# Kernel optimization log

Measured on AMD Instinct MI355X. Metric: run time of the kernel, lower is better.

## Reference

```python
import jax, jax.numpy as jnp
import numpy as np

B, S, D, H = 4, 2048, 1024, 16
DK = D // H

def setup_inputs() -> dict:
    key = jax.random.key(0)
    ks = jax.random.split(key, 11)
    s = 1.0 / np.sqrt(D)
    inp = {
        'q': jax.random.normal(ks[0], (B, S, D), jnp.float32),
        'k': jax.random.normal(ks[1], (B, S, D), jnp.float32),
        'v': jax.random.normal(ks[2], (B, S, D), jnp.float32),
        'Wq': jax.random.normal(ks[3], (D, D), jnp.float32) * s,
        'bq': jnp.zeros((D,), jnp.float32),
        'Wk': jax.random.normal(ks[4], (D, D), jnp.float32) * s,
        'bk': jnp.zeros((D,), jnp.float32),
        'Wv': jax.random.normal(ks[5], (D, D), jnp.float32) * s,
        'bv': jnp.zeros((D,), jnp.float32),
        'Wo': jax.random.normal(ks[6], (D, D), jnp.float32) * s,
        'bo': jnp.zeros((D,), jnp.float32),
    }
    return inp

def reference(q, k, v, Wq, bq, Wk, bk, Wv, bv, Wo, bo):
    # torch Linear: x @ W.T + b
    def proj(x, W, b):
        # [B,S,D] -> [B,H,S,DK]
        y = jnp.einsum('bsd,ed->bse', x, W) + b
        return y.reshape(B, S, H, DK).transpose(0, 2, 1, 3)
    qh, kh, vh = proj(q, Wq, bq), proj(k, Wk, bk), proj(v, Wv, bv)
    scores = jnp.einsum('bhqd,bhkd->bhqk', qh, kh) / jnp.sqrt(jnp.float32(DK))
    attn = jax.nn.softmax(scores, axis=-1)  # dropout p=0.0 (eval)
    out = jnp.einsum('bhqk,bhkd->bhqd', attn, vh)
    concat = out.transpose(0, 2, 1, 3).reshape(B, S, D)
    return jnp.einsum('bsd,ed->bse', concat, Wo) + bo
```

## Files before the change

kernel.cpp:

```cpp
#include <hip/hip_runtime.h>
#include <hip/hip_bf16.h>
#include <cstdint>

#define BB 4
#define SS 2048
#define DD 1024
#define HH 16
#define DKH 64

using bf16x8  = __attribute__((ext_vector_type(8))) __bf16;
using f32x4   = __attribute__((ext_vector_type(4))) float;
using ushort8 = __attribute__((ext_vector_type(8))) unsigned short;

__device__ __forceinline__ unsigned short f2bf(float f) {
  unsigned int u = __builtin_bit_cast(unsigned int, f);
  u += 0x7fffu + ((u >> 16) & 1u);
  return (unsigned short)(u >> 16);
}

__device__ __forceinline__ void gload16(const void* g, void* l) {
  __builtin_amdgcn_global_load_lds(
      (const __attribute__((address_space(1))) void*)g,
      (__attribute__((address_space(3))) void*)l,
      16, 0, 0);
}

__global__ __launch_bounds__(256) void cvt_one(const float* __restrict__ s,
                                               unsigned short* __restrict__ d) {
  const int i = ((int)blockIdx.x * 256 + (int)threadIdx.x) * 8;
  const float4* p = reinterpret_cast<const float4*>(s + i);
  float4 x = p[0], y = p[1];
  ushort8 r;
  r[0] = f2bf(x.x); r[1] = f2bf(x.y); r[2] = f2bf(x.z); r[3] = f2bf(x.w);
  r[4] = f2bf(y.x); r[5] = f2bf(y.y); r[6] = f2bf(y.z); r[7] = f2bf(y.w);
  *reinterpret_cast<ushort8*>(d + i) = r;
}

struct CvtW {
  const float* src[4];
  unsigned short* dst[4];
};
__global__ __launch_bounds__(256) void cvt_w(CvtW a) {
  const int b = blockIdx.x, seg = b >> 9, boff = b & 511;
  const float* s = a.src[seg];
  unsigned short* d = a.dst[seg];
  const int i = (boff * 256 + (int)threadIdx.x) * 8;
  const float4* p = reinterpret_cast<const float4*>(s + i);
  float4 x = p[0], y = p[1];
  ushort8 r;
  r[0] = f2bf(x.x); r[1] = f2bf(x.y); r[2] = f2bf(x.z); r[3] = f2bf(x.w);
  r[4] = f2bf(y.x); r[5] = f2bf(y.y); r[6] = f2bf(y.z); r[7] = f2bf(y.w);
  *reinterpret_cast<ushort8*>(d + i) = r;
}

__global__ __launch_bounds__(256) void gemm_bt(const unsigned short* __restrict__ A,
                                               const unsigned short* __restrict__ Bt,
                                               const float* __restrict__ bias,
                                               void* __restrict__ Cout,
                                               int M, int N, int K, int out_f32) {
  __shared__ alignas(16) unsigned short As[128 * 32];
  __shared__ alignas(16) unsigned short Bs[128 * 32];
  const int lid = blockIdx.x;
  const int swz = (lid & 7) * 64 + (lid >> 3);
  const int bx = swz >> 3, by = swz & 7;
  const int tid = threadIdx.x;
  const int wid = tid >> 6, lane = tid & 63;
  const int lg = lane >> 4, li = lane & 15;
  const int row0 = bx * 128, col0 = by * 128;
  const int wr = (wid >> 1) * 64, wc = (wid & 1) * 64;

  f32x4 acc[4][4] = {};

  const int c1 = tid, c2 = tid + 256;
  const size_t aoff1 = (size_t)(row0 + (c1 >> 2)) * K + ((c1 & 3) * 8);
  const size_t aoff2 = (size_t)(row0 + (c2 >> 2)) * K + ((c2 & 3) * 8);
  const size_t boff1 = (size_t)(col0 + (c1 >> 2)) * K + ((c1 & 3) * 8);
  const size_t boff2 = (size_t)(col0 + (c2 >> 2)) * K + ((c2 & 3) * 8);
  char* asb = (char*)As; char* bsb = (char*)Bs;
  char* a_dst1 = asb + wid * 1024;
  char* a_dst2 = asb + 4096 + wid * 1024;
  char* b_dst1 = bsb + wid * 1024;
  char* b_dst2 = bsb + 4096 + wid * 1024;

  for (int k0 = 0; k0 < K; k0 += 32) {
    gload16(A + aoff1 + k0, a_dst1);
    gload16(A + aoff2 + k0, a_dst2);
    gload16(Bt + boff1 + k0, b_dst1);
    gload16(Bt + boff2 + k0, b_dst2);
    __syncthreads();
    bf16x8 af[4], bfr[4];
#pragma unroll
    for (int i = 0; i < 4; i++) {
      af[i]  = *reinterpret_cast<const bf16x8*>(&As[(wr + i * 16 + li) * 32 + lg * 8]);
      bfr[i] = *reinterpret_cast<const bf16x8*>(&Bs[(wc + i * 16 + li) * 32 + lg * 8]);
    }
#pragma unroll
    for (int mi = 0; mi < 4; mi++)
#pragma unroll
      for (int ni = 0; ni < 4; ni++)
        acc[mi][ni] = __builtin_amdgcn_mfma_f32_16x16x32_bf16(af[mi], bfr[ni], acc[mi][ni], 0, 0, 0);
    __syncthreads();
  }

#pragma unroll
  for (int ni = 0; ni < 4; ni++) {
    const int col = col0 + wc + ni * 16 + li;
    const float bv = bias[col];
#pragma unroll
    for (int mi = 0; mi < 4; mi++) {
#pragma unroll
      for (int j = 0; j < 4; j++) {
        const int row = row0 + wr + mi * 16 + lg * 4 + j;
        const float val = acc[mi][ni][j] + bv;
        if (out_f32) ((float*)Cout)[(size_t)row * N + col] = val;
        else ((unsigned short*)Cout)[(size_t)row * N + col] = f2bf(val);
      }
    }
  }
}

__global__ __launch_bounds__(256) void attn(const unsigned short* __restrict__ Qp,
                                            const unsigned short* __restrict__ Kp,
                                            const unsigned short* __restrict__ Vp,
                                            unsigned short* __restrict__ Oc) {
  const int lid = blockIdx.x;
  const int swz = (lid & 7) * 256 + (lid >> 3);
  const int bh = swz >> 5;
  const int b = bh >> 4, h = bh & 15;
  const int q0 = (swz & 31) * 64;
  const int tid = threadIdx.x;
  const int wid = tid >> 6, lane = tid & 63;
  const int lg = lane >> 4, li = lane & 15;

  __shared__ alignas(16) unsigned short Ks[2][64 * 64];
  __shared__ alignas(16) unsigned short Vt[64][72];
  __shared__ alignas(16) unsigned short Pb[4][16][72];

  const size_t base = ((size_t)b * SS) * DD + h * DKH;
  const unsigned short* Qb = Qp + base;
  const unsigned short* Kb = Kp + base;
  const unsigned short* Vb = Vp + base;

  const int qrow = q0 + wid * 16 + li;
  const bf16x8 qf0 = *reinterpret_cast<const bf16x8*>(Qb + (size_t)qrow * DD + lg * 8);
  const bf16x8 qf1 = *reinterpret_cast<const bf16x8*>(Qb + (size_t)qrow * DD + 32 + lg * 8);

  f32x4 acc[4] = {};
  float mrow[4] = {-1e30f, -1e30f, -1e30f, -1e30f};
  float lrow[4] = {0.f, 0.f, 0.f, 0.f};

  const int vkey = tid & 63, vdk = (tid >> 6) * 16;

  const int c0 = tid, c1 = tid + 256;
  const int r0c = c0 >> 3, r1c = c1 >> 3;
  const size_t koff0 = (size_t)r0c * DD + (((c0 & 7) ^ (r0c & 7)) * 8);
  const size_t koff1 = (size_t)r1c * DD + (((c1 & 7) ^ (r1c & 7)) * 8);
  char* ksb = (char*)Ks;
  char* kdst0 = ksb + wid * 1024;
  char* kdst1 = ksb + 4096 + wid * 1024;

  gload16(Kb + koff0, kdst0);
  gload16(Kb + koff1, kdst1);
  __syncthreads();
  int buf = 0;

  const int swk = li & 7;

  for (int kv0 = 0; kv0 < SS; kv0 += 64) {
    if (kv0 + 64 < SS) {
      const int nb = buf ^ 1;
      gload16(Kb + (size_t)(kv0 + 64) * DD + koff0, kdst0 + nb * 8192);
      gload16(Kb + (size_t)(kv0 + 64) * DD + koff1, kdst1 + nb * 8192);
    }

    ushort8 v0 = *reinterpret_cast<const ushort8*>(Vb + (size_t)(kv0 + vkey) * DD + vdk);
    ushort8 v1 = *reinterpret_cast<const ushort8*>(Vb + (size_t)(kv0 + vkey) * DD + vdk + 8);

    f32x4 sc[4];
#pragma unroll
    for (int n = 0; n < 4; n++) {
      const unsigned short* krow = &Ks[buf][(n * 16 + li) * 64];
      bf16x8 kb0 = *reinterpret_cast<const bf16x8*>(&krow[(lg ^ swk) * 8]);
      bf16x8 kb1 = *reinterpret_cast<const bf16x8*>(&krow[((lg + 4) ^ swk) * 8]);
      f32x4 c = {};
      c = __builtin_amdgcn_mfma_f32_16x16x32_bf16(qf0, kb0, c, 0, 0, 0);
      c = __builtin_amdgcn_mfma_f32_16x16x32_bf16(qf1, kb1, c, 0, 0, 0);
      sc[n] = c;
    }

    float pvv[4][4]; float alpha[4];
#pragma unroll
    for (int j = 0; j < 4; j++) {
      float mx = fmaxf(fmaxf(sc[0][j], sc[1][j]), fmaxf(sc[2][j], sc[3][j]));
      mx = fmaxf(mx, __shfl_xor(mx, 1, 16));
      mx = fmaxf(mx, __shfl_xor(mx, 2, 16));
      mx = fmaxf(mx, __shfl_xor(mx, 4, 16));
      mx = fmaxf(mx, __shfl_xor(mx, 8, 16));
      mx *= 0.125f;
      const float mnew = fmaxf(mrow[j], mx);
      alpha[j] = __expf(mrow[j] - mnew);
      float ps = 0.f;
#pragma unroll
      for (int n = 0; n < 4; n++) {
        const float p = __expf(sc[n][j] * 0.125f - mnew);
        pvv[n][j] = p; ps += p;
      }
      ps += __shfl_xor(ps, 1, 16);
      ps += __shfl_xor(ps, 2, 16);
      ps += __shfl_xor(ps, 4, 16);
      ps += __shfl_xor(ps, 8, 16);
      lrow[j] = lrow[j] * alpha[j] + ps;
      mrow[j] = mnew;
    }

    __syncthreads();
#pragma unroll
    for (int i = 0; i < 8; i++) {
      Vt[vdk + i][vkey] = v0[i];
      Vt[vdk + 8 + i][vkey] = v1[i];
    }
#pragma unroll
    for (int n = 0; n < 4; n++)
#pragma unroll
      for (int j = 0; j < 4; j++)
        Pb[wid][lg * 4 + j][n * 16 + li] = f2bf(pvv[n][j]);
#pragma unroll
    for (int n = 0; n < 4; n++)
#pragma unroll
      for (int j = 0; j < 4; j++)
        acc[n][j] *= alpha[j];
    __syncthreads();

    const bf16x8 pf0 = *reinterpret_cast<const bf16x8*>(&Pb[wid][li][lg * 8]);
    const bf16x8 pf1 = *reinterpret_cast<const bf16x8*>(&Pb[wid][li][32 + lg * 8]);
#pragma unroll
    for (int n = 0; n < 4; n++) {
      bf16x8 vb0 = *reinterpret_cast<const bf16x8*>(&Vt[n * 16 + li][lg * 8]);
      bf16x8 vb1 = *reinterpret_cast<const bf16x8*>(&Vt[n * 16 + li][32 + lg * 8]);
      acc[n] = __builtin_amdgcn_mfma_f32_16x16x32_bf16(pf0, vb0, acc[n], 0, 0, 0);
      acc[n] = __builtin_amdgcn_mfma_f32_16x16x32_bf16(pf1, vb1, acc[n], 0, 0, 0);
    }
    buf ^= 1;
  }

  float inv[4];
#pragma unroll
  for (int j = 0; j < 4; j++) inv[j] = 1.0f / lrow[j];
  unsigned short* Ob = Oc + base;
#pragma unroll
  for (int n = 0; n < 4; n++)
#pragma unroll
    for (int j = 0; j < 4; j++) {
      const int r = q0 + wid * 16 + lg * 4 + j;
      Ob[(size_t)r * DD + n * 16 + li] = f2bf(acc[n][j] * inv[j]);
    }
}

extern "C" void kernel_launch(void* const* d_in, const int* in_sizes, int n_in,
                              void* d_out, int out_size, void* d_ws, size_t ws_size,
                              hipStream_t stream) {
  const float* q  = (const float*)d_in[0];
  const float* k  = (const float*)d_in[1];
  const float* v  = (const float*)d_in[2];
  const float* Wq = (const float*)d_in[3];
  const float* bq = (const float*)d_in[4];
  const float* Wk = (const float*)d_in[5];
  const float* bk = (const float*)d_in[6];
  const float* Wv = (const float*)d_in[7];
  const float* bv = (const float*)d_in[8];
  const float* Wo = (const float*)d_in[9];
  const float* bo = (const float*)d_in[10];
  float* out = (float*)d_out;

  const size_t NE = (size_t)BB * SS * DD;
  const size_t WE = (size_t)DD * DD;
  unsigned short* ws  = (unsigned short*)d_ws;
  unsigned short* ab  = ws;
  unsigned short* Qp  = ab + NE;
  unsigned short* Kp  = Qp + NE;
  unsigned short* Vp  = Kp + NE;
  unsigned short* Wqb = Vp + NE;
  unsigned short* Wkb = Wqb + WE;
  unsigned short* Wvb = Wkb + WE;
  unsigned short* Wob = Wvb + WE;
  (void)ws_size; (void)in_sizes; (void)n_in; (void)out_size;

  CvtW cw;
  cw.src[0] = Wq; cw.dst[0] = Wqb;
  cw.src[1] = Wk; cw.dst[1] = Wkb;
  cw.src[2] = Wv; cw.dst[2] = Wvb;
  cw.src[3] = Wo; cw.dst[3] = Wob;
  cvt_w<<<2048, 256, 0, stream>>>(cw);

  cvt_one<<<4096, 256, 0, stream>>>(q, ab);
  gemm_bt<<<512, 256, 0, stream>>>(ab, Wqb, bq, Qp, 8192, 1024, 1024, 0);
  cvt_one<<<4096, 256, 0, stream>>>(k, ab);
  gemm_bt<<<512, 256, 0, stream>>>(ab, Wkb, bk, Kp, 8192, 1024, 1024, 0);
  cvt_one<<<4096, 256, 0, stream>>>(v, ab);
  gemm_bt<<<512, 256, 0, stream>>>(ab, Wvb, bv, Vp, 8192, 1024, 1024, 0);

  attn<<<2048, 256, 0, stream>>>(Qp, Kp, Vp, ab);

  gemm_bt<<<512, 256, 0, stream>>>(ab, Wob, bo, out, 8192, 1024, 1024, 1);
}
```

Baseline: 522.8 us.

## Double-buffer GEMM LDS tiles, lazy softmax rescale, packed bf16 convert

The projection GEMM now double-buffers its A/B LDS tiles, issuing the next k-slice's global-to-LDS loads before computing on the current one. This is meant to hide global load latency and removes one barrier per iteration. In attention, the running max is updated only when the new max exceeds the old by more than 8, so the accumulator rescale is skipped via a wave-wide vote in most iterations. P is converted to bf16 with packed v_cvt_pk_bf16_f32 instructions instead of manual rounding. The lazy rescale lets exp values reach up to e^8 before rescaling, which the fp32 accumulators can tolerate but which changes bf16 rounding behaviour slightly.

```diff
diff --git a/kernel.cpp b/kernel.cpp
--- a/kernel.cpp
+++ b/kernel.cpp
@@ -58,8 +58,8 @@
                                                const float* __restrict__ bias,
                                                void* __restrict__ Cout,
                                                int M, int N, int K, int out_f32) {
-  __shared__ alignas(16) unsigned short As[128 * 32];
-  __shared__ alignas(16) unsigned short Bs[128 * 32];
+  __shared__ alignas(16) unsigned short As[2][128 * 32];
+  __shared__ alignas(16) unsigned short Bs[2][128 * 32];
   const int lid = blockIdx.x;
   const int swz = (lid & 7) * 64 + (lid >> 3);
   const int bx = swz >> 3, by = swz & 7;
@@ -82,17 +82,28 @@
   char* b_dst1 = bsb + wid * 1024;
   char* b_dst2 = bsb + 4096 + wid * 1024;
 
+  gload16(A + aoff1, a_dst1);
+  gload16(A + aoff2, a_dst2);
+  gload16(Bt + boff1, b_dst1);
+  gload16(Bt + boff2, b_dst2);
+  __syncthreads();
+  int cur = 0;
+
   for (int k0 = 0; k0 < K; k0 += 32) {
-    gload16(A + aoff1 + k0, a_dst1);
-    gload16(A + aoff2 + k0, a_dst2);
-    gload16(Bt + boff1 + k0, b_dst1);
-    gload16(Bt + boff2 + k0, b_dst2);
-    __syncthreads();
+    if (k0 + 32 < K) {
+      const int nb = (cur ^ 1) * 8192;
+      gload16(A + aoff1 + k0 + 32, a_dst1 + nb);
+      gload16(A + aoff2 + k0 + 32, a_dst2 + nb);
+      gload16(Bt + boff1 + k0 + 32, b_dst1 + nb);
+      gload16(Bt + boff2 + k0 + 32, b_dst2 + nb);
+    }
+    const unsigned short* Ab = As[cur];
+    const unsigned short* Bb = Bs[cur];
     bf16x8 af[4], bfr[4];
 #pragma unroll
     for (int i = 0; i < 4; i++) {
-      af[i]  = *reinterpret_cast<const bf16x8*>(&As[(wr + i * 16 + li) * 32 + lg * 8]);
-      bfr[i] = *reinterpret_cast<const bf16x8*>(&Bs[(wc + i * 16 + li) * 32 + lg * 8]);
+      af[i]  = *reinterpret_cast<const bf16x8*>(&Ab[(wr + i * 16 + li) * 32 + lg * 8]);
+      bfr[i] = *reinterpret_cast<const bf16x8*>(&Bb[(wc + i * 16 + li) * 32 + lg * 8]);
     }
 #pragma unroll
     for (int mi = 0; mi < 4; mi++)
@@ -100,6 +111,7 @@
       for (int ni = 0; ni < 4; ni++)
         acc[mi][ni] = __builtin_amdgcn_mfma_f32_16x16x32_bf16(af[mi], bfr[ni], acc[mi][ni], 0, 0, 0);
     __syncthreads();
+    cur ^= 1;
   }
 
 #pragma unroll
@@ -188,7 +200,8 @@
       sc[n] = c;
     }
 
-    float pvv[4][4]; float alpha[4];
+    float pvv[4][4]; float alf[4];
+    int growAny = 0;
 #pragma unroll
     for (int j = 0; j < 4; j++) {
       float mx = fmaxf(fmaxf(sc[0][j], sc[1][j]), fmaxf(sc[2][j], sc[3][j]));
@@ -197,20 +210,24 @@
       mx = fmaxf(mx, __shfl_xor(mx, 4, 16));
       mx = fmaxf(mx, __shfl_xor(mx, 8, 16));
       mx *= 0.125f;
-      const float mnew = fmaxf(mrow[j], mx);
-      alpha[j] = __expf(mrow[j] - mnew);
+      float a = 1.0f;
+      if (mx > mrow[j] + 8.0f) {
+        a = __expf(mrow[j] - mx);
+        mrow[j] = mx;
+        growAny = 1;
+      }
+      alf[j] = a;
       float ps = 0.f;
 #pragma unroll
       for (int n = 0; n < 4; n++) {
-        const float p = __expf(sc[n][j] * 0.125f - mnew);
+        const float p = __expf(sc[n][j] * 0.125f - mrow[j]);
         pvv[n][j] = p; ps += p;
       }
       ps += __shfl_xor(ps, 1, 16);
       ps += __shfl_xor(ps, 2, 16);
       ps += __shfl_xor(ps, 4, 16);
       ps += __shfl_xor(ps, 8, 16);
-      lrow[j] = lrow[j] * alpha[j] + ps;
-      mrow[j] = mnew;
+      lrow[j] = lrow[j] * a + ps;
     }
 
     __syncthreads();
@@ -220,15 +237,23 @@
       Vt[vdk + 8 + i][vkey] = v1[i];
     }
 #pragma unroll
-    for (int n = 0; n < 4; n++)
-#pragma unroll
-      for (int j = 0; j < 4; j++)
-        Pb[wid][lg * 4 + j][n * 16 + li] = f2bf(pvv[n][j]);
-#pragma unroll
-    for (int n = 0; n < 4; n++)
-#pragma unroll
-      for (int j = 0; j < 4; j++)
-        acc[n][j] *= alpha[j];
+    for (int j = 0; j < 4; j++) {
+      unsigned int r01, r23;
+      asm("v_cvt_pk_bf16_f32 %0, %1, %2" : "=v"(r01) : "v"(pvv[0][j]), "v"(pvv[1][j]));
+      asm("v_cvt_pk_bf16_f32 %0, %1, %2" : "=v"(r23) : "v"(pvv[2][j]), "v"(pvv[3][j]));
+      unsigned short* pr = &Pb[wid][lg * 4 + j][li];
+      pr[0]  = (unsigned short)(r01 & 0xffffu);
+      pr[16] = (unsigned short)(r01 >> 16);
+      pr[32] = (unsigned short)(r23 & 0xffffu);
+      pr[48] = (unsigned short)(r23 >> 16);
+    }
+    if (__any(growAny)) {
+#pragma unroll
+      for (int n = 0; n < 4; n++)
+#pragma unroll
+        for (int j = 0; j < 4; j++)
+          acc[n][j] *= alf[j];
+    }
     __syncthreads();
 
     const bf16x8 pf0 = *reinterpret_cast<const bf16x8*>(&Pb[wid][li][lg * 8]);
```

New measurement: 501.2 us. -4.1%, faster.
